# Optimization experiments

Hardware: AMD Instinct MI355X
Metric: run time of the kernel (lower is better)

## Reference

```python
import jax, jax.numpy as jnp
import numpy as np

B, T, D = 1, 2048, 4096
N_HEADS, KV_HEADS, HEAD_DIM = 32, 8, 128
WINDOW = 1024
ROPE_THETA = 500000.0
EPS = 1e-6
LARGE_NEGATIVE = np.finfo(np.float32).min


def _rms_norm(x, w, eps=EPS):
    xf = x.astype(jnp.float32)
    out = xf * jax.lax.rsqrt(jnp.square(xf).mean(-1, keepdims=True) + eps)
    return (w.astype(jnp.float32) * out).astype(x.dtype)


def _positions_from_segment_ids(seg_ids):
    t = seg_ids.shape[1]
    return jax.vmap(lambda row: jnp.where(row != 0, jnp.arange(t) - jnp.argmax(row), 2 ** 30))(seg_ids)


def _rope_sin_cos(positions, head_dim=HEAD_DIM, theta=ROPE_THETA):
    fraction = jnp.arange(0, head_dim, 2, dtype=jnp.float32) / head_dim
    inv_freq = 1.0 / (theta ** fraction)
    sinusoid = jnp.einsum('BT,k->BTk', positions.astype(jnp.float32), inv_freq)
    return jnp.sin(sinusoid), jnp.cos(sinusoid)


def _apply_rope(x, sin, cos):
    half = x.shape[-1] // 2
    x1, x2 = x[..., :half], x[..., half:]
    sin, cos = sin[:, :, None, :], cos[:, :, None, :]
    return jnp.concatenate([x1 * cos - x2 * sin, x2 * cos + x1 * sin], axis=-1).astype(x.dtype)


def setup_inputs() -> dict:
    key = jax.random.key(0)
    ks = jax.random.split(key, 6)
    wscale = 1.0 / np.sqrt(D)
    return {
        'x': jax.random.normal(ks[0], (B, T, D), dtype=jnp.float32),
        'Wq': jax.random.normal(ks[1], (D, N_HEADS * HEAD_DIM), dtype=jnp.float32) * wscale,
        'Wk': jax.random.normal(ks[2], (D, KV_HEADS * HEAD_DIM), dtype=jnp.float32) * wscale,
        'Wv': jax.random.normal(ks[3], (D, KV_HEADS * HEAD_DIM), dtype=jnp.float32) * wscale,
        'Wo': jax.random.normal(ks[4], (N_HEADS * HEAD_DIM, D), dtype=jnp.float32) * wscale,
        'q_norm_w': jnp.ones((N_HEADS * HEAD_DIM,), dtype=jnp.float32),
        'k_norm_w': jnp.ones((KV_HEADS * HEAD_DIM,), dtype=jnp.float32),
        'segment_ids': jnp.ones((B, T), dtype=jnp.int32),
    }


def reference(x, Wq, Wk, Wv, Wo, q_norm_w, k_norm_w, segment_ids):
    b, t, _ = x.shape
    positions = _positions_from_segment_ids(segment_ids)
    sin, cos = _rope_sin_cos(positions)

    # QKV projections; q/k RMS-normed over the flattened (heads*head_dim) axis pre-reshape.
    q = _rms_norm(x @ Wq, q_norm_w).reshape(b, t, N_HEADS, HEAD_DIM)
    k = _rms_norm(x @ Wk, k_norm_w).reshape(b, t, KV_HEADS, HEAD_DIM)
    v = (x @ Wv).reshape(b, t, KV_HEADS, HEAD_DIM)

    q = _apply_rope(q, sin, cos)
    k = _apply_rope(k, sin, cos)

    # GQA: physically repeat kv heads (repeat_kv in source).
    n_rep = N_HEADS // KV_HEADS
    k = jnp.repeat(k[:, :, :, None, :], n_rep, axis=3).reshape(b, t, N_HEADS, HEAD_DIM)
    v = jnp.repeat(v[:, :, :, None, :], n_rep, axis=3).reshape(b, t, N_HEADS, HEAD_DIM)

    # causal + sliding-window + same-segment mask, [B, T, S]
    i = positions[:, :, None]
    j = positions[:, None, :]
    same_seg = segment_ids[:, :, None] == segment_ids[:, None, :]
    mask = (j <= i) & ((i - j) < WINDOW) & same_seg & (segment_ids != 0)[:, None, :]

    scale = HEAD_DIM ** -0.5
    logits = jnp.einsum('BTNH,BSNH->BNTS', q, k) * jnp.array(scale, dtype=q.dtype)
    padded = jnp.where(mask[:, None, :, :], logits.astype(jnp.float32), LARGE_NEGATIVE)
    probs = jax.nn.softmax(padded, axis=-1).astype(k.dtype)
    attn = jnp.einsum('BNTS,BSNH->BTNH', probs, v)
    return attn.reshape(b, t, N_HEADS * HEAD_DIM) @ Wo
```

## Files before the change

kernel.cpp:

```cpp
#include <hip/hip_runtime.h>
#include <cstdint>
#include <cstddef>

typedef __bf16 bf16_t;
typedef __bf16 bf16x8 __attribute__((ext_vector_type(8)));
typedef __bf16 bf16x4 __attribute__((ext_vector_type(4)));
typedef __bf16 bf16x2 __attribute__((ext_vector_type(2)));
typedef float f32x4 __attribute__((ext_vector_type(4)));

#define T_LEN 2048
#define DMODEL 4096
#define NHEADS 32
#define KVHEADS 8
#define HD 128
#define QD 4096
#define KD 1024
#define QKVD 6144
#define WIN 1024
#define VS 72

__global__ void pos_kernel(const int* __restrict__ seg, int* __restrict__ positions) {
  __shared__ int svals[256], sidx[256];
  int tid = threadIdx.x;
  int bestv = -2147483647 - 1, besti = 0;
  for (int t = tid; t < T_LEN; t += 256) {
    int v = seg[t];
    if (v > bestv) { bestv = v; besti = t; }
  }
  svals[tid] = bestv; sidx[tid] = besti;
  __syncthreads();
  for (int st = 128; st > 0; st >>= 1) {
    if (tid < st) {
      if (svals[tid+st] > svals[tid] || (svals[tid+st] == svals[tid] && sidx[tid+st] < sidx[tid])) {
        svals[tid] = svals[tid+st]; sidx[tid] = sidx[tid+st];
      }
    }
    __syncthreads();
  }
  int amax = sidx[0];
  for (int t = tid; t < T_LEN; t += 256)
    positions[t] = (seg[t] != 0) ? (t - amax) : (1 << 30);
}

__global__ void sincos_kernel(const int* __restrict__ positions, float* __restrict__ sc) {
  int t = blockIdx.x, i = threadIdx.x;
  float inv = expf(-(float)i * (logf(500000.0f) / 64.0f));
  float ang = (float)positions[t] * inv;
  sc[(t*64 + i)*2 + 0] = sinf(ang);
  sc[(t*64 + i)*2 + 1] = cosf(ang);
}

__global__ void cvt_kernel(const float* __restrict__ in, bf16_t* __restrict__ out, int n) {
  int i = (blockIdx.x * blockDim.x + threadIdx.x) * 8;
  if (i >= n) return;
  float4 a = *(const float4*)(in + i);
  float4 b = *(const float4*)(in + i + 4);
  bf16x8 o;
  o[0]=(bf16_t)a.x; o[1]=(bf16_t)a.y; o[2]=(bf16_t)a.z; o[3]=(bf16_t)a.w;
  o[4]=(bf16_t)b.x; o[5]=(bf16_t)b.y; o[6]=(bf16_t)b.z; o[7]=(bf16_t)b.w;
  *(bf16x8*)(out + i) = o;
}

__global__ void transcvt_kernel(const float* __restrict__ W, bf16_t* __restrict__ Wt, int K, int N) {
  __shared__ float tile[32][33];
  int tx = threadIdx.x, ty = threadIdx.y;
  int bx = blockIdx.x, by = blockIdx.y;
  #pragma unroll
  for (int i = 0; i < 4; i++) {
    int k = by*32 + ty + i*8;
    tile[ty + i*8][tx] = W[(size_t)k * N + bx*32 + tx];
  }
  __syncthreads();
  int t = ty*32 + tx;
  int n = t >> 3;
  int kq = t & 7;
  bf16x4 v;
  #pragma unroll
  for (int e = 0; e < 4; e++) v[e] = (bf16_t)tile[kq*4 + e][n];
  *(bf16x4*)(Wt + (size_t)(bx*32 + n) * K + by*32 + kq*4) = v;
}

__device__ __forceinline__ void gld_lds16(const void* g, void* l) {
  __builtin_amdgcn_global_load_lds((__attribute__((address_space(1))) void*)g,
                                   (__attribute__((address_space(3))) void*)l, 16, 0, 0);
}

__global__ __launch_bounds__(512, 2) void gemm192_kernel(
    const bf16_t* __restrict__ A, const bf16_t* __restrict__ Bt,
    bf16_t* __restrict__ Cb, int M, int N, int K, int NBM) {
  __shared__ bf16_t As[2 * 256 * 64];
  __shared__ bf16_t Bs[2 * 192 * 64];
  int tid = threadIdx.x;
  int w = tid >> 6, l = tid & 63, lr = l & 15, lg = l >> 4;
  int wr = w >> 2, wc = w & 3;
  int nwg = gridDim.x;
  int wg  = blockIdx.x;
  int cpx = nwg >> 3;
  int swz = (wg & 7) * cpx + (wg >> 3);
  int bm = swz % NBM, bn = swz / NBM;
  const int NT = K >> 6;

  auto stageA = [&](int tt, int h) {
    int b2 = tt & 1;
    bf16_t* ldsb = As + b2*16384 + h*8192;
    #pragma unroll
    for (int r2 = 0; r2 < 2; r2++) {
      int L = r2*8192 + tid*16;
      int row = L >> 7;
      int chunk = (L >> 4) & 7;
      int scn = chunk ^ (row & 7);
      gld_lds16(A + ((size_t)bm*256 + h*128 + row) * K + tt*64 + scn*8,
                ldsb + r2*4096 + w*512);
    }
  };
  auto stageB = [&](int tt, int u) {
    int b2 = tt & 1;
    bf16_t* ldsb = Bs + b2*12288 + u*4096;
    int row = tid >> 3;
    int scn = (tid & 7) ^ (row & 7);
    gld_lds16(Bt + ((size_t)bn*192 + u*64 + row) * K + tt*64 + scn*8,
              ldsb + w*512);
  };
  auto afrag = [&](int b2, int row, int kk) -> bf16x8 {
    int chunk = (kk*4 + lg) ^ (row & 7);
    return *(const bf16x8*)((const char*)(As + b2*16384) + row*128 + chunk*16);
  };
  auto bfrag = [&](int b2, int row, int kk) -> bf16x8 {
    int chunk = (kk*4 + lg) ^ (row & 7);
    return *(const bf16x8*)((const char*)(Bs + b2*12288) + row*128 + chunk*16);
  };

  f32x4 acc[8][3] = {};
  bf16x8 a[8][2], bb[3][2];

  stageA(0, 0); stageA(0, 1); stageB(0, 0); stageB(0, 1); stageB(0, 2);
  stageA(1, 0); stageA(1, 1); stageB(1, 0); stageB(1, 1);
  asm volatile("s_waitcnt vmcnt(6)" ::: "memory");
  __builtin_amdgcn_s_barrier();

  for (int t = 0; t < NT; t++) {
    int b = t & 1;
    #pragma unroll
    for (int fm = 0; fm < 8; fm++)
      #pragma unroll
      for (int kk = 0; kk < 2; kk++)
        a[fm][kk] = afrag(b, wr*128 + fm*16 + lr, kk);
    #pragma unroll
    for (int fn = 0; fn < 2; fn++)
      #pragma unroll
      for (int kk = 0; kk < 2; kk++)
        bb[fn][kk] = bfrag(b, wc*48 + fn*16 + lr, kk);
    if (t + 1 < NT) stageB(t + 1, 2);
    __builtin_amdgcn_s_barrier();
    asm volatile("s_waitcnt lgkmcnt(0)" ::: "memory");
    __builtin_amdgcn_s_setprio(1);
    #pragma unroll
    for (int fm = 0; fm < 4; fm++)
      #pragma unroll
      for (int fn = 0; fn < 2; fn++)
        #pragma unroll
        for (int kk = 0; kk < 2; kk++)
          acc[fm][fn] = __builtin_amdgcn_mfma_f32_16x16x32_bf16(a[fm][kk], bb[fn][kk], acc[fm][fn], 0, 0, 0);
    __builtin_amdgcn_s_setprio(0);
    __builtin_amdgcn_s_barrier();
    #pragma unroll
    for (int kk = 0; kk < 2; kk++)
      bb[2][kk] = bfrag(b, wc*48 + 32 + lr, kk);
    if (t + 2 < NT) stageA(t + 2, 0);
    __builtin_amdgcn_s_barrier();
    asm volatile("s_waitcnt lgkmcnt(0)" ::: "memory");
    __builtin_amdgcn_s_setprio(1);
    #pragma unroll
    for (int fm = 0; fm < 4; fm++)
      #pragma unroll
      for (int kk = 0; kk < 2; kk++)
        acc[fm][2] = __builtin_amdgcn_mfma_f32_16x16x32_bf16(a[fm][kk], bb[2][kk], acc[fm][2], 0, 0, 0);
    __builtin_amdgcn_s_setprio(0);
    __builtin_amdgcn_s_barrier();
    if (t + 2 < NT) stageA(t + 2, 1);
    __builtin_amdgcn_s_barrier();
    __builtin_amdgcn_s_setprio(1);
    #pragma unroll
    for (int fm = 4; fm < 8; fm++)
      #pragma unroll
      for (int kk = 0; kk < 2; kk++)
        acc[fm][2] = __builtin_amdgcn_mfma_f32_16x16x32_bf16(a[fm][kk], bb[2][kk], acc[fm][2], 0, 0, 0);
    __builtin_amdgcn_s_setprio(0);
    __builtin_amdgcn_s_barrier();
    if (t + 2 < NT) { stageB(t + 2, 0); stageB(t + 2, 1); }
    __builtin_amdgcn_s_barrier();
    __builtin_amdgcn_s_setprio(1);
    #pragma unroll
    for (int fm = 4; fm < 8; fm++)
      #pragma unroll
      for (int fn = 0; fn < 2; fn++)
        #pragma unroll
        for (int kk = 0; kk < 2; kk++)
          acc[fm][fn] = __builtin_amdgcn_mfma_f32_16x16x32_bf16(a[fm][kk], bb[fn][kk], acc[fm][fn], 0, 0, 0);
    __builtin_amdgcn_s_setprio(0);
    if (t < NT - 2) asm volatile("s_waitcnt vmcnt(6)" ::: "memory");
    else            asm volatile("s_waitcnt vmcnt(0)" ::: "memory");
    __builtin_amdgcn_s_barrier();
  }

  #pragma unroll
  for (int fm = 0; fm < 8; fm++) {
    #pragma unroll
    for (int fn = 0; fn < 3; fn++) {
      #pragma unroll
      for (int r2 = 0; r2 < 4; r2++) {
        int row = bm*256 + wr*128 + fm*16 + lg*4 + r2;
        int col = bn*192 + wc*48 + fn*16 + lr;
        Cb[(size_t)row * N + col] = (bf16_t)acc[fm][fn][r2];
      }
    }
  }
}

#define MFMA_QUAD(FM0, FN0)                                                     \
  { _Pragma("unroll") for (int fm_ = 0; fm_ < QFM; fm_++)                        \
    _Pragma("unroll") for (int fn_ = 0; fn_ < 2; fn_++)                          \
    _Pragma("unroll") for (int kk_ = 0; kk_ < 2; kk_++)                          \
      acc[(FM0)+fm_][(FN0)+fn_] = __builtin_amdgcn_mfma_f32_16x16x32_bf16(       \
          a[(FM0)+fm_][kk_], bb[(FN0)+fn_][kk_], acc[(FM0)+fm_][(FN0)+fn_], 0,0,0); }

template<bool WRITE_BF16, int AM>
__global__ __launch_bounds__(512, 2) void gemm256_kernel(
    const bf16_t* __restrict__ A, const bf16_t* __restrict__ Bt,
    bf16_t* __restrict__ Cb, float* __restrict__ Cf,
    int M, int N, int K, int NBM) {
  constexpr int BM  = AM * 128;
  constexpr int NH  = AM + 2;
  constexpr int FM2 = AM * 4;
  constexpr int QFM = AM * 2;
  __shared__ bf16_t As[2 * BM * 64];
  __shared__ bf16_t Bs[2 * 256 * 64];
  int tid = threadIdx.x;
  int w = tid >> 6, l = tid & 63, lr = l & 15, lg = l >> 4;
  int wr = w >> 2, wc = w & 3;
  int nwg = gridDim.x;
  int wg  = blockIdx.x;
  int cpx = nwg >> 3;
  int swz = (wg & 7) * cpx + (wg >> 3);
  int bm = swz % NBM, bn = swz / NBM;
  const int NT = K >> 6;

  auto stage = [&](int tt, int h) {
    int b2 = tt & 1;
    const bf16_t* G; size_t grow0; bf16_t* ldsb;
    if (h < AM) { G = A;  grow0 = (size_t)bm*BM + h*128;        ldsb = As + b2*(BM*64) + h*8192; }
    else        { G = Bt; grow0 = (size_t)bn*256 + (h-AM)*128;  ldsb = Bs + b2*16384 + (h-AM)*8192; }
    int kcol = tt * 64;
    #pragma unroll
    for (int r2 = 0; r2 < 2; r2++) {
      int L = r2*8192 + tid*16;
      int row = L >> 7;
      int chunk = (L >> 4) & 7;
      int scn = chunk ^ (row & 7);
      gld_lds16(G + (grow0 + (size_t)row) * K + kcol + scn*8,
                ldsb + r2*4096 + w*512);
    }
  };
  auto afrag = [&](int b2, int row, int kk) -> bf16x8 {
    int chunk = (kk*4 + lg) ^ (row & 7);
    return *(const bf16x8*)((const char*)(As + b2*(BM*64)) + row*128 + chunk*16);
  };
  auto bfrag = [&](int b2, int row, int kk) -> bf16x8 {
    int chunk = (kk*4 + lg) ^ (row & 7);
    return *(const bf16x8*)((const char*)(Bs + b2*16384) + row*128 + chunk*16);
  };

  f32x4 acc[FM2][4] = {};
  bf16x8 a[FM2][2], bb[4][2];

  #pragma unroll
  for (int h = 0; h < NH; h++) stage(0, h);
  #pragma unroll
  for (int h = 0; h < NH - 1; h++) stage(1, h);
  if constexpr (AM == 2) asm volatile("s_waitcnt vmcnt(6)" ::: "memory");
  else                   asm volatile("s_waitcnt vmcnt(4)" ::: "memory");
  __builtin_amdgcn_s_barrier();

  for (int t = 0; t < NT; t++) {
    int b = t & 1;
    #pragma unroll
    for (int fm = 0; fm < FM2; fm++)
      #pragma unroll
      for (int kk = 0; kk < 2; kk++)
        a[fm][kk] = afrag(b, wr*(BM/2) + fm*16 + lr, kk);
    #pragma unroll
    for (int fn = 0; fn < 2; fn++)
      #pragma unroll
      for (int kk = 0; kk < 2; kk++)
        bb[fn][kk] = bfrag(b, wc*64 + fn*16 + lr, kk);
    if (t + 1 < NT) stage(t + 1, NH - 1);
    __builtin_amdgcn_s_barrier();
    asm volatile("s_waitcnt lgkmcnt(0)" ::: "memory");
    __builtin_amdgcn_s_setprio(1);
    MFMA_QUAD(0, 0);
    __builtin_amdgcn_s_setprio(0);
    __builtin_amdgcn_s_barrier();
    #pragma unroll
    for (int fn = 2; fn < 4; fn++)
      #pragma unroll
      for (int kk = 0; kk < 2; kk++)
        bb[fn][kk] = bfrag(b, wc*64 + fn*16 + lr, kk);
    if (t + 2 < NT) stage(t + 2, 0);
    __builtin_amdgcn_s_barrier();
    asm volatile("s_waitcnt lgkmcnt(0)" ::: "memory");
    __builtin_amdgcn_s_setprio(1);
    MFMA_QUAD(0, 2);
    __builtin_amdgcn_s_setprio(0);
    __builtin_amdgcn_s_barrier();
    if (t + 2 < NT) stage(t + 2, 1);
    __builtin_amdgcn_s_barrier();
    __builtin_amdgcn_s_setprio(1);
    MFMA_QUAD(QFM, 2);
    __builtin_amdgcn_s_setprio(0);
    __builtin_amdgcn_s_barrier();
    if constexpr (AM == 2) { if (t + 2 < NT) stage(t + 2, 2); }
    __builtin_amdgcn_s_barrier();
    __builtin_amdgcn_s_setprio(1);
    MFMA_QUAD(QFM, 0);
    __builtin_amdgcn_s_setprio(0);
    if (t < NT - 2) {
      if constexpr (AM == 2) asm volatile("s_waitcnt vmcnt(6)" ::: "memory");
      else                   asm volatile("s_waitcnt vmcnt(4)" ::: "memory");
    } else {
      asm volatile("s_waitcnt vmcnt(0)" ::: "memory");
    }
    __builtin_amdgcn_s_barrier();
  }

  #pragma unroll
  for (int fm = 0; fm < FM2; fm++) {
    #pragma unroll
    for (int fn = 0; fn < 4; fn++) {
      #pragma unroll
      for (int r2 = 0; r2 < 4; r2++) {
        int row = bm*BM + wr*(BM/2) + fm*16 + lg*4 + r2;
        int col = bn*256 + wc*64 + fn*16 + lr;
        if (WRITE_BF16) Cb[(size_t)row * N + col] = (bf16_t)acc[fm][fn][r2];
        else            Cf[(size_t)row * N + col] = acc[fm][fn][r2];
      }
    }
  }
}

__global__ __launch_bounds__(256) void normrope_kernel(bf16_t* __restrict__ qkv,
    const float* __restrict__ qw, const float* __restrict__ kw,
    const float* __restrict__ sc) {
  int t = blockIdx.x;
  int tid = threadIdx.x;
  bf16_t* qrow = qkv + (size_t)t * QKVD;
  bf16_t* krow = qrow + QD;
  __shared__ float red[8];
  float s = 0.f;
  {
    const bf16x8* p = (const bf16x8*)(qrow + tid*16);
    bf16x8 v0 = p[0], v1 = p[1];
    #pragma unroll
    for (int j = 0; j < 8; j++) { float a = (float)v0[j], b = (float)v1[j]; s += a*a + b*b; }
  }
  #pragma unroll
  for (int o = 32; o; o >>= 1) s += __shfl_xor(s, o);
  if ((tid & 63) == 0) red[tid >> 6] = s;
  float sk = 0.f;
  {
    bf16x4 v = *(const bf16x4*)(krow + tid*4);
    #pragma unroll
    for (int j = 0; j < 4; j++) { float a = (float)v[j]; sk += a*a; }
  }
  #pragma unroll
  for (int o = 32; o; o >>= 1) sk += __shfl_xor(sk, o);
  if ((tid & 63) == 0) red[4 + (tid >> 6)] = sk;
  __syncthreads();
  float rq = rsqrtf((red[0]+red[1]+red[2]+red[3]) / (float)QD + 1e-6f);
  float rk = rsqrtf((red[4]+red[5]+red[6]+red[7]) / (float)KD + 1e-6f);
  const float ascale = 0.08838834764831845f;
  for (int p = tid; p < 2048; p += 256) {
    int hh = p >> 6, i = p & 63;
    int i1 = hh*HD + i, i2 = i1 + 64;
    float x1 = (float)qrow[i1] * rq * qw[i1];
    float x2 = (float)qrow[i2] * rq * qw[i2];
    float sn = sc[(t*64 + i)*2 + 0], cs = sc[(t*64 + i)*2 + 1];
    qrow[i1] = (bf16_t)((x1*cs - x2*sn) * ascale);
    qrow[i2] = (bf16_t)((x2*cs + x1*sn) * ascale);
  }
  for (int p = tid; p < 512; p += 256) {
    int hh = p >> 6, i = p & 63;
    int i1 = hh*HD + i, i2 = i1 + 64;
    float x1 = (float)krow[i1] * rk * kw[i1];
    float x2 = (float)krow[i2] * rk * kw[i2];
    float sn = sc[(t*64 + i)*2 + 0], cs = sc[(t*64 + i)*2 + 1];
    krow[i1] = (bf16_t)(x1*cs - x2*sn);
    krow[i2] = (bf16_t)(x2*cs + x1*sn);
  }
}

__global__ __launch_bounds__(512, 3) void attn_kernel(const bf16_t* __restrict__ qkv,
    const int* __restrict__ positions, const int* __restrict__ seg,
    bf16_t* __restrict__ O) {
  __shared__ bf16_t Ks[64 * HD];
  __shared__ bf16_t Vt[HD * VS];
  __shared__ bf16_t P[8][16 * VS];
  int tid = threadIdx.x;
  int w = tid >> 6, l = tid & 63, lr = l & 15, lg = l >> 4;
  int qb = blockIdx.x * 128;
  int h = blockIdx.y;
  int kvh = h >> 2;
  int q0 = qb + w * 16;
  const bf16_t* Kg = qkv + QD + (size_t)kvh * HD;
  const bf16_t* Vg = qkv + QD + KD + (size_t)kvh * HD;

  bf16x8 qf[4];
  {
    const bf16_t* Qrow = qkv + (size_t)(q0 + lr) * QKVD + h * HD;
    #pragma unroll
    for (int c = 0; c < 4; c++) qf[c] = *(const bf16x8*)(Qrow + c*32 + lg*8);
  }
  int pos_i[4], seg_i[4];
  #pragma unroll
  for (int r = 0; r < 4; r++) { int i = q0 + lg*4 + r; pos_i[r] = positions[i]; seg_i[r] = seg[i]; }
  f32x4 o[8] = {};
  float m[4], lsum[4];
  #pragma unroll
  for (int r = 0; r < 4; r++) { m[r] = -__builtin_inff(); lsum[r] = 0.f; }

  int vkp = tid & 31, vdg = tid >> 5;
  bf16x8 vrA, vrB;

  auto issueK = [&](int j0) {
    #pragma unroll
    for (int i = 0; i < 2; i++) {
      int c = tid + i*512;
      int row = c >> 4;
      int scn = (c & 15) ^ (row & 7);
      gld_lds16(Kg + (size_t)(j0 + row) * QKVD + scn*8,
                (char*)Ks + (size_t)(i*512 + (tid & 448))*16);
    }
  };
  auto loadV = [&](int j0) {
    const bf16_t* vp = Vg + (size_t)(j0 + 2*vkp) * QKVD + vdg*8;
    vrA = *(const bf16x8*)vp;
    vrB = *(const bf16x8*)(vp + QKVD);
  };

  int jstart = qb - (WIN - 1); if (jstart < 0) jstart = 0; jstart &= ~63;
  const int jlast = qb + 64;
  loadV(jstart);
  issueK(jstart);

  for (int j0 = jstart; j0 <= jlast; j0 += 64) {
    #pragma unroll
    for (int e = 0; e < 8; e++) {
      bf16x2 pr; pr[0] = vrA[e]; pr[1] = vrB[e];
      *(bf16x2*)(Vt + (vdg*8 + e)*VS + 2*vkp) = pr;
    }
    int pj[4], sj[4];
    #pragma unroll
    for (int kt = 0; kt < 4; kt++) { int j = j0 + kt*16 + lr; pj[kt] = positions[j]; sj[kt] = seg[j]; }
    asm volatile("" ::: "memory");
    if (j0 + 64 <= jlast) loadV(j0 + 64);
    asm volatile("" ::: "memory");
    asm volatile("s_waitcnt vmcnt(2) lgkmcnt(0)" ::: "memory");
    __builtin_amdgcn_s_barrier();

    bool active = (j0 <= q0 + 15) && (j0 + 63 >= q0 - (WIN - 1));
    if (active) {
      f32x4 s[4] = {};
      __builtin_amdgcn_s_setprio(1);
      #pragma unroll
      for (int kt = 0; kt < 4; kt++) {
        int row = kt*16 + lr;
        const char* kb = (const char*)Ks + row*256;
        #pragma unroll
        for (int c = 0; c < 4; c++) {
          bf16x8 kf = *(const bf16x8*)(kb + (((c*4 + lg) ^ (row & 7)) * 16));
          s[kt] = __builtin_amdgcn_mfma_f32_16x16x32_bf16(qf[c], kf, s[kt], 0, 0, 0);
        }
      }
      __builtin_amdgcn_s_setprio(0);
      #pragma unroll
      for (int kt = 0; kt < 4; kt++) {
        #pragma unroll
        for (int r = 0; r < 4; r++) {
          bool valid = (pj[kt] <= pos_i[r]) && (pos_i[r] - pj[kt] < WIN) && (seg_i[r] == sj[kt]) && (sj[kt] != 0);
          s[kt][r] = valid ? s[kt][r] : -__builtin_inff();
        }
      }
      #pragma unroll
      for (int r = 0; r < 4; r++) {
        float smax = fmaxf(fmaxf(s[0][r], s[1][r]), fmaxf(s[2][r], s[3][r]));
        if (__any(smax > m[r] + 8.f)) {
          float rm = smax;
          #pragma unroll
          for (int o2 = 1; o2 < 16; o2 <<= 1) rm = fmaxf(rm, __shfl_xor(rm, o2));
          if (rm > m[r] + 8.f) {
            float rescale = __expf(m[r] - rm);
            lsum[r] *= rescale;
            #pragma unroll
            for (int n = 0; n < 8; n++) o[n][r] *= rescale;
            m[r] = rm;
          }
        }
        float mub = fmaxf(m[r], -1e37f);
        float p0 = __expf(s[0][r] - mub);
        float p1 = __expf(s[1][r] - mub);
        float p2 = __expf(s[2][r] - mub);
        float p3 = __expf(s[3][r] - mub);
        lsum[r] += (p0 + p1) + (p2 + p3);
        int prow = (lg*4 + r) * VS;
        P[w][prow + lr]      = (bf16_t)p0;
        P[w][prow + 16 + lr] = (bf16_t)p1;
        P[w][prow + 32 + lr] = (bf16_t)p2;
        P[w][prow + 48 + lr] = (bf16_t)p3;
      }
    }
    __builtin_amdgcn_s_barrier();
    asm volatile("" ::: "memory");

    if (j0 + 64 <= jlast) issueK(j0 + 64);
    if (active) {
      __builtin_amdgcn_s_setprio(1);
      #pragma unroll
      for (int ks = 0; ks < 2; ks++) {
        bf16x8 pa = *(const bf16x8*)(&P[w][lr*VS + ks*32 + lg*8]);
        #pragma unroll
        for (int n = 0; n < 8; n++) {
          bf16x8 vb = *(const bf16x8*)(&Vt[(n*16 + lr)*VS + ks*32 + lg*8]);
          o[n] = __builtin_amdgcn_mfma_f32_16x16x32_bf16(pa, vb, o[n], 0, 0, 0);
        }
      }
      __builtin_amdgcn_s_setprio(0);
    }
    __builtin_amdgcn_s_barrier();
  }
  #pragma unroll
  for (int r = 0; r < 4; r++) {
    float ls = lsum[r];
    #pragma unroll
    for (int o2 = 1; o2 < 16; o2 <<= 1) ls += __shfl_xor(ls, o2);
    float inv = ls > 0.f ? 1.f / ls : 0.f;
    int row = q0 + lg*4 + r;
    #pragma unroll
    for (int n = 0; n < 8; n++)
      O[(size_t)row * QD + h*HD + n*16 + lr] = (bf16_t)(o[n][r] * inv);
  }
}

extern "C" void kernel_launch(void* const* d_in, const int* in_sizes, int n_in,
                              void* d_out, int out_size, void* d_ws, size_t ws_size,
                              hipStream_t stream) {
  (void)in_sizes; (void)n_in; (void)out_size; (void)ws_size;
  const float* x  = (const float*)d_in[0];
  const float* Wq = (const float*)d_in[1];
  const float* Wk = (const float*)d_in[2];
  const float* Wv = (const float*)d_in[3];
  const float* Wo = (const float*)d_in[4];
  const float* qw = (const float*)d_in[5];
  const float* kw = (const float*)d_in[6];
  const int*  seg = (const int*)d_in[7];
  float* out = (float*)d_out;

  char* base = (char*)d_ws;
  size_t off = 0;
  auto alloc = [&](size_t b) { void* r = base + off; off = (off + b + 255) & ~(size_t)255; return r; };
  bf16_t* xb    = (bf16_t*)alloc((size_t)T_LEN * DMODEL * 2);
  bf16_t* Wallt = (bf16_t*)alloc((size_t)QKVD * DMODEL * 2);
  bf16_t* Wot   = (bf16_t*)alloc((size_t)DMODEL * QD * 2);
  bf16_t* qkv   = (bf16_t*)alloc((size_t)T_LEN * QKVD * 2);
  int*    posi  = (int*)alloc((size_t)T_LEN * 4);
  float*  sc    = (float*)alloc((size_t)T_LEN * 64 * 2 * 4);
  bf16_t* ao    = xb;

  pos_kernel<<<1, 256, 0, stream>>>(seg, posi);
  sincos_kernel<<<T_LEN, 64, 0, stream>>>(posi, sc);
  cvt_kernel<<<(T_LEN * DMODEL / 8 + 255) / 256, 256, 0, stream>>>(x, xb, T_LEN * DMODEL);
  transcvt_kernel<<<dim3(QD/32, DMODEL/32), dim3(32, 8), 0, stream>>>(Wq, Wallt, DMODEL, QD);
  transcvt_kernel<<<dim3(KD/32, DMODEL/32), dim3(32, 8), 0, stream>>>(Wk, Wallt + (size_t)QD * DMODEL, DMODEL, KD);
  transcvt_kernel<<<dim3(KD/32, DMODEL/32), dim3(32, 8), 0, stream>>>(Wv, Wallt + (size_t)(QD + KD) * DMODEL, DMODEL, KD);
  transcvt_kernel<<<dim3(DMODEL/32, QD/32), dim3(32, 8), 0, stream>>>(Wo, Wot, QD, DMODEL);
  gemm192_kernel<<<dim3((T_LEN/256)*(QKVD/192)), 512, 0, stream>>>(
      xb, Wallt, qkv, T_LEN, QKVD, DMODEL, T_LEN/256);
  normrope_kernel<<<T_LEN, 256, 0, stream>>>(qkv, qw, kw, sc);
  attn_kernel<<<dim3(T_LEN/128, NHEADS), 512, 0, stream>>>(qkv, posi, seg, ao);
  gemm256_kernel<false, 1><<<dim3((T_LEN/128)*(DMODEL/256)), 512, 0, stream>>>(
      ao, Wot, nullptr, out, T_LEN, DMODEL, QD, T_LEN/128);
}
```

Baseline: 360.9 us.

## Halve QKV GEMM M-tile to 128 and reverse attention block order

The QKV projection GEMM tile drops from 256x192 to 128x192. That doubles the grid from 256 to 512 workgroups so more of the GPU is busy at once. The software pipeline is reworked to match: smaller A staging, three MFMA phases per k-step, and adjusted vmcnt waits. Separately, the attention kernel walks query blocks in reverse, so the later blocks, which have more work under the causal sliding window, start first and load balances better. In exchange, each GEMM block reuses the B tile across fewer rows, so total operand traffic goes up.

```diff
diff --git a/kernel.cpp b/kernel.cpp
--- a/kernel.cpp
+++ b/kernel.cpp
@@ -85,10 +85,10 @@
                                    (__attribute__((address_space(3))) void*)l, 16, 0, 0);
 }
 
-__global__ __launch_bounds__(512, 2) void gemm192_kernel(
+__global__ __launch_bounds__(512, 2) void gemm1_kernel(
     const bf16_t* __restrict__ A, const bf16_t* __restrict__ Bt,
     bf16_t* __restrict__ Cb, int M, int N, int K, int NBM) {
-  __shared__ bf16_t As[2 * 256 * 64];
+  __shared__ bf16_t As[2 * 128 * 64];
   __shared__ bf16_t Bs[2 * 192 * 64];
   int tid = threadIdx.x;
   int w = tid >> 6, l = tid & 63, lr = l & 15, lg = l >> 4;
@@ -101,21 +101,14 @@
   const int NT = K >> 6;
 
   auto stageA = [&](int tt, int h) {
-    int b2 = tt & 1;
-    bf16_t* ldsb = As + b2*16384 + h*8192;
-    #pragma unroll
-    for (int r2 = 0; r2 < 2; r2++) {
-      int L = r2*8192 + tid*16;
-      int row = L >> 7;
-      int chunk = (L >> 4) & 7;
-      int scn = chunk ^ (row & 7);
-      gld_lds16(A + ((size_t)bm*256 + h*128 + row) * K + tt*64 + scn*8,
-                ldsb + r2*4096 + w*512);
-    }
+    bf16_t* ldsb = As + (tt & 1)*8192 + h*4096;
+    int row = tid >> 3;
+    int scn = (tid & 7) ^ (row & 7);
+    gld_lds16(A + ((size_t)bm*128 + h*64 + row) * K + tt*64 + scn*8,
+              ldsb + w*512);
   };
   auto stageB = [&](int tt, int u) {
-    int b2 = tt & 1;
-    bf16_t* ldsb = Bs + b2*12288 + u*4096;
+    bf16_t* ldsb = Bs + (tt & 1)*12288 + u*4096;
     int row = tid >> 3;
     int scn = (tid & 7) ^ (row & 7);
     gld_lds16(Bt + ((size_t)bn*192 + u*64 + row) * K + tt*64 + scn*8,
@@ -123,93 +116,85 @@
   };
   auto afrag = [&](int b2, int row, int kk) -> bf16x8 {
     int chunk = (kk*4 + lg) ^ (row & 7);
-    return *(const bf16x8*)((const char*)(As + b2*16384) + row*128 + chunk*16);
+    return *(const bf16x8*)((const char*)(As + b2*8192) + row*128 + chunk*16);
   };
   auto bfrag = [&](int b2, int row, int kk) -> bf16x8 {
     int chunk = (kk*4 + lg) ^ (row & 7);
     return *(const bf16x8*)((const char*)(Bs + b2*12288) + row*128 + chunk*16);
   };
 
-  f32x4 acc[8][3] = {};
-  bf16x8 a[8][2], bb[3][2];
+  f32x4 acc[4][3] = {};
+  bf16x8 a[4][2], bb[3][2];
 
   stageA(0, 0); stageA(0, 1); stageB(0, 0); stageB(0, 1); stageB(0, 2);
   stageA(1, 0); stageA(1, 1); stageB(1, 0); stageB(1, 1);
-  asm volatile("s_waitcnt vmcnt(6)" ::: "memory");
+  asm volatile("s_waitcnt vmcnt(4)" ::: "memory");
   __builtin_amdgcn_s_barrier();
 
   for (int t = 0; t < NT; t++) {
     int b = t & 1;
     #pragma unroll
-    for (int fm = 0; fm < 8; fm++)
+    for (int fm = 0; fm < 4; fm++)
       #pragma unroll
       for (int kk = 0; kk < 2; kk++)
-        a[fm][kk] = afrag(b, wr*128 + fm*16 + lr, kk);
-    #pragma unroll
-    for (int fn = 0; fn < 2; fn++)
+        a[fm][kk] = afrag(b, wr*64 + fm*16 + lr, kk);
+    #pragma unroll
+    for (int kk = 0; kk < 2; kk++)
+      bb[0][kk] = bfrag(b, wc*48 + lr, kk);
+    if (t + 1 < NT) stageB(t + 1, 2);
+    __builtin_amdgcn_s_barrier();
+    asm volatile("s_waitcnt lgkmcnt(0)" ::: "memory");
+    __builtin_amdgcn_s_setprio(1);
+    #pragma unroll
+    for (int fm = 0; fm < 4; fm++)
       #pragma unroll
       for (int kk = 0; kk < 2; kk++)
-        bb[fn][kk] = bfrag(b, wc*48 + fn*16 + lr, kk);
-    if (t + 1 < NT) stageB(t + 1, 2);
+        acc[fm][0] = __builtin_amdgcn_mfma_f32_16x16x32_bf16(a[fm][kk], bb[0][kk], acc[fm][0], 0, 0, 0);
+    __builtin_amdgcn_s_setprio(0);
+    __builtin_amdgcn_s_barrier();
+    #pragma unroll
+    for (int kk = 0; kk < 2; kk++)
+      bb[1][kk] = bfrag(b, wc*48 + 16 + lr, kk);
+    if (t + 2 < NT) { stageA(t + 2, 0); stageA(t + 2, 1); }
     __builtin_amdgcn_s_barrier();
     asm volatile("s_waitcnt lgkmcnt(0)" ::: "memory");
     __builtin_amdgcn_s_setprio(1);
     #pragma unroll
     for (int fm = 0; fm < 4; fm++)
       #pragma unroll
-      for (int fn = 0; fn < 2; fn++)
-        #pragma unroll
-        for (int kk = 0; kk < 2; kk++)
-          acc[fm][fn] = __builtin_amdgcn_mfma_f32_16x16x32_bf16(a[fm][kk], bb[fn][kk], acc[fm][fn], 0, 0, 0);
+      for (int kk = 0; kk < 2; kk++)
+        acc[fm][1] = __builtin_amdgcn_mfma_f32_16x16x32_bf16(a[fm][kk], bb[1][kk], acc[fm][1], 0, 0, 0);
     __builtin_amdgcn_s_setprio(0);
     __builtin_amdgcn_s_barrier();
     #pragma unroll
     for (int kk = 0; kk < 2; kk++)
       bb[2][kk] = bfrag(b, wc*48 + 32 + lr, kk);
-    if (t + 2 < NT) stageA(t + 2, 0);
     __builtin_amdgcn_s_barrier();
     asm volatile("s_waitcnt lgkmcnt(0)" ::: "memory");
     __builtin_amdgcn_s_setprio(1);
     #pragma unroll
     for (int fm = 0; fm < 4; fm++)
-      #pragma unroll
-      for (int kk = 0; kk < 2; kk++)
-        acc[fm][2] = __builtin_amdgcn_mfma_f32_16x16x32_bf16(a[fm][kk], bb[2][kk], acc[fm][2], 0, 0, 0);
-    __builtin_amdgcn_s_setprio(0);
-    __builtin_amdgcn_s_barrier();
-    if (t + 2 < NT) stageA(t + 2, 1);
-    __builtin_amdgcn_s_barrier();
-    __builtin_amdgcn_s_setprio(1);
-    #pragma unroll
-    for (int fm = 4; fm < 8; fm++)
-      #pragma unroll
-      for (int kk = 0; kk < 2; kk++)
-        acc[fm][2] = __builtin_amdgcn_mfma_f32_16x16x32_bf16(a[fm][kk], bb[2][kk], acc[fm][2], 0, 0, 0);
+      acc[fm][2] = __builtin_amdgcn_mfma_f32_16x16x32_bf16(a[fm][0], bb[2][0], acc[fm][2], 0, 0, 0);
     __builtin_amdgcn_s_setprio(0);
     __builtin_amdgcn_s_barrier();
     if (t + 2 < NT) { stageB(t + 2, 0); stageB(t + 2, 1); }
-    __builtin_amdgcn_s_barrier();
-    __builtin_amdgcn_s_setprio(1);
-    #pragma unroll
-    for (int fm = 4; fm < 8; fm++)
-      #pragma unroll
-      for (int fn = 0; fn < 2; fn++)
-        #pragma unroll
-        for (int kk = 0; kk < 2; kk++)
-          acc[fm][fn] = __builtin_amdgcn_mfma_f32_16x16x32_bf16(a[fm][kk], bb[fn][kk], acc[fm][fn], 0, 0, 0);
-    __builtin_amdgcn_s_setprio(0);
-    if (t < NT - 2) asm volatile("s_waitcnt vmcnt(6)" ::: "memory");
+    __builtin_amdgcn_s_setprio(1);
+    #pragma unroll
+    for (int fm = 0; fm < 4; fm++)
+      acc[fm][2] = __builtin_amdgcn_mfma_f32_16x16x32_bf16(a[fm][1], bb[2][1], acc[fm][2], 0, 0, 0);
+    __builtin_amdgcn_s_setprio(0);
+    if (t < NT - 2) asm volatile("s_waitcnt vmcnt(4)" ::: "memory");
     else            asm volatile("s_waitcnt vmcnt(0)" ::: "memory");
     __builtin_amdgcn_s_barrier();
   }
 
   #pragma unroll
-  for (int fm = 0; fm < 8; fm++) {
+  for (int fm = 0; fm < 4; fm++) {
     #pragma unroll
     for (int fn = 0; fn < 3; fn++) {
       #pragma unroll
       for (int r2 = 0; r2 < 4; r2++) {
-        int row = bm*256 + wr*128 + fm*16 + lg*4 + r2;
+        int row = bm*128 + wr*64 + fm*16 + lg*4 + r2;
         int col = bn*192 + wc*48 + fn*16 + lr;
         Cb[(size_t)row * N + col] = (bf16_t)acc[fm][fn][r2];
       }
@@ -406,7 +391,7 @@
   __shared__ bf16_t P[8][16 * VS];
   int tid = threadIdx.x;
   int w = tid >> 6, l = tid & 63, lr = l & 15, lg = l >> 4;
-  int qb = blockIdx.x * 128;
+  int qb = (gridDim.x - 1 - blockIdx.x) * 128;
   int h = blockIdx.y;
   int kvh = h >> 2;
   int q0 = qb + w * 16;
@@ -581,8 +566,8 @@
   transcvt_kernel<<<dim3(KD/32, DMODEL/32), dim3(32, 8), 0, stream>>>(Wk, Wallt + (size_t)QD * DMODEL, DMODEL, KD);
   transcvt_kernel<<<dim3(KD/32, DMODEL/32), dim3(32, 8), 0, stream>>>(Wv, Wallt + (size_t)(QD + KD) * DMODEL, DMODEL, KD);
   transcvt_kernel<<<dim3(DMODEL/32, QD/32), dim3(32, 8), 0, stream>>>(Wo, Wot, QD, DMODEL);
-  gemm192_kernel<<<dim3((T_LEN/256)*(QKVD/192)), 512, 0, stream>>>(
-      xb, Wallt, qkv, T_LEN, QKVD, DMODEL, T_LEN/256);
+  gemm1_kernel<<<dim3((T_LEN/128)*(QKVD/192)), 512, 0, stream>>>(
+      xb, Wallt, qkv, T_LEN, QKVD, DMODEL, T_LEN/128);
   normrope_kernel<<<T_LEN, 256, 0, stream>>>(qkv, qw, kw, sc);
   attn_kernel<<<dim3(T_LEN/128, NHEADS), 512, 0, stream>>>(qkv, posi, seg, ao);
   gemm256_kernel<false, 1><<<dim3((T_LEN/128)*(DMODEL/256)), 512, 0, stream>>>(
```

Result: no change. 358.5 us (-0.7%).
